# Performance work log

Measured on AMD Instinct MI355X. Metric: run time of the kernel, lower is better.

## Reference

```python
import jax, jax.numpy as jnp
import numpy as np

N_NODES = 50000
N_EDGES = 800000
HIDDEN = 128
EPS = 1e-5


def _layernorm(x, g, b):
    m = jnp.mean(x, axis=-1, keepdims=True)
    v = jnp.var(x, axis=-1, keepdims=True)
    return (x - m) / jnp.sqrt(v + EPS) * g + b


def _batchnorm(x, g, b):
    # training-mode BatchNorm1d: stats over the node (batch) axis, biased var
    m = jnp.mean(x, axis=0, keepdims=True)
    v = jnp.var(x, axis=0, keepdims=True)
    return (x - m) / jnp.sqrt(v + EPS) * g + b


def _instnorm(x):
    # torch InstanceNorm1d on a 2D [N,C] input: unbatched (C,L) view ->
    # normalize each row over the feature axis, no affine params
    m = jnp.mean(x, axis=-1, keepdims=True)
    v = jnp.var(x, axis=-1, keepdims=True)
    return (x - m) / jnp.sqrt(v + EPS)


def _gcn_conv(x, W, b, row, col, norm, n):
    # PyG GCNConv: out[col] += norm * (x @ W)[row]; + bias
    xw = x @ W
    msgs = xw[row] * norm[:, None]          # [E+N, H]
    out = jax.ops.segment_sum(msgs, col, num_segments=n)
    return out + b


def setup_inputs() -> dict:
    key = jax.random.key(0)
    ks = jax.random.split(key, 12)
    H = HIDDEN
    x = jax.random.normal(ks[0], (N_NODES, 2), dtype=jnp.float32)
    edge_index = jax.random.randint(ks[1], (2, N_EDGES), 0, N_NODES, dtype=jnp.int64)

    def lin(k, fan_in, shape):
        bound = 1.0 / np.sqrt(fan_in)
        return jax.random.uniform(k, shape, jnp.float32, -bound, bound)

    inp = {
        "x": x,
        "edge_index": edge_index,
        "coord_W": lin(ks[2], 2, (2, H)),
        "coord_b": lin(ks[3], 2, (H,)),
        "ln_g": jnp.ones((H,), jnp.float32),
        "ln_b": jnp.zeros((H,), jnp.float32),
        "bn_g": jnp.ones((H,), jnp.float32),
        "bn_b": jnp.zeros((H,), jnp.float32),
        "W1": lin(ks[4], H, (H, H)),
        "b1": jnp.zeros((H,), jnp.float32),
        "W2": lin(ks[5], H, (H, H)),
        "b2": jnp.zeros((H,), jnp.float32),
        "W3": lin(ks[6], H, (H, H)),
        "b3": jnp.zeros((H,), jnp.float32),
        "fc1_W": lin(ks[7], H, (H, 32)),
        "fc1_b": lin(ks[8], H, (32,)),
        "fc2_W": lin(ks[9], 32, (32, 2)),
        "fc2_b": lin(ks[10], 32, (2,)),
    }
    return inp


def reference(x, edge_index, coord_W, coord_b, ln_g, ln_b, bn_g, bn_b,
              W1, b1, W2, b2, W3, b3, fc1_W, fc1_b, fc2_W, fc2_b):
    n = x.shape[0]
    loop = jnp.arange(n, dtype=edge_index.dtype)
    row = jnp.concatenate([edge_index[0], loop])
    col = jnp.concatenate([edge_index[1], loop])
    deg = jax.ops.segment_sum(jnp.ones_like(col, dtype=x.dtype), col, num_segments=n)
    dinv = 1.0 / jnp.sqrt(deg)              # deg >= 1 thanks to self-loops
    norm = dinv[row] * dinv[col]

    h = jax.nn.relu(x @ coord_W + coord_b)
    h = _layernorm(h, ln_g, ln_b)

    for W, b in ((W1, b1), (W2, b2), (W3, b3)):
        identity = h
        h = jax.nn.relu(_gcn_conv(h, W, b, row, col, norm, n))
        h = _batchnorm(h, bn_g, bn_b)
        h = _instnorm(h + identity)

    h = jax.nn.relu(h @ fc1_W + fc1_b)
    return jnp.tanh(h @ fc2_W + fc2_b)
```

## Files before the change

kernel.cpp:

```cpp
#include <hip/hip_runtime.h>
#include <hip/hip_bf16.h>
#include <hip/hip_fp16.h>
#include <stdint.h>

#define NN 50000
#define NE 800000
#define HD 128
#define EPSN 1e-5f
#define CAP 1152000
#define NCLS 49
#define NSB 196

typedef __hip_bfloat16 bf16;
typedef __attribute__((ext_vector_type(8))) _Float16 half8;
typedef __attribute__((ext_vector_type(4))) float f32x4;

__device__ __forceinline__ float us2f(unsigned short u) { return __uint_as_float((uint32_t)u << 16); }
__device__ __forceinline__ ushort f2us(float f) {
    bf16 b = __float2bfloat16(f);
    return *reinterpret_cast<ushort*>(&b);
}
__device__ __forceinline__ ushort f2h(float f) {
    __half h = __float2half(f);
    return *reinterpret_cast<ushort*>(&h);
}
__device__ __forceinline__ float h2f(ushort u) {
    __half h = *reinterpret_cast<__half*>(&u);
    return __half2float(h);
}

__device__ __forceinline__ void cvt8(float4 v, float* o) {
    uint32_t a = __float_as_uint(v.x), b = __float_as_uint(v.y);
    uint32_t c = __float_as_uint(v.z), d = __float_as_uint(v.w);
    o[0] = h2f((ushort)(a & 0xffff)); o[1] = h2f((ushort)(a >> 16));
    o[2] = h2f((ushort)(b & 0xffff)); o[3] = h2f((ushort)(b >> 16));
    o[4] = h2f((ushort)(c & 0xffff)); o[5] = h2f((ushort)(c >> 16));
    o[6] = h2f((ushort)(d & 0xffff)); o[7] = h2f((ushort)(d >> 16));
}

#define O_X    0
#define O_CW   100000
#define O_CB   100256
#define O_LNG  100384
#define O_LNB  100512
#define O_BNG  100640
#define O_BNB  100768
#define O_W1   100896
#define O_B1   117280
#define O_W2   117408
#define O_B2   133792
#define O_W3   133920
#define O_B3   150304
#define O_F1W  150432
#define O_F1B  154528
#define O_F2W  154560
#define O_F2B  154624
#define O_TOT  154626

struct Ptrs { const void* p[17]; };

__device__ const int SEG_OFF[18] = {O_X, O_CW, O_CB, O_LNG, O_LNB, O_BNG, O_BNB,
                                    O_W1, O_B1, O_W2, O_B2, O_W3, O_B3,
                                    O_F1W, O_F1B, O_F2W, O_F2B, O_TOT};

__device__ __forceinline__ int eidx(const int* __restrict__ ei, int isL, int which, int e) {
    size_t base = (size_t)which * NE + e;
    return isL ? ei[2 * base] : ei[base];
}

__global__ void k_detect(const int* __restrict__ ei, const ushort* __restrict__ cw,
                         int* __restrict__ flags) {
    int t = threadIdx.x;
    int v = ei[2 * t + 1] | ei[1000000 + 2 * t + 1];
    int bad = 0;
    if (t < 128) {
        float val = us2f(cw[2 * t]);
        bad = !(fabsf(val) <= 1.0f);
    }
    for (int o = 32; o; o >>= 1) { v |= __shfl_xor(v, o); bad |= __shfl_xor(bad, o); }
    __shared__ int sv[4], sb[4];
    if ((t & 63) == 0) { sv[t >> 6] = v; sb[t >> 6] = bad; }
    __syncthreads();
    if (t == 0) {
        flags[0] = ((sv[0] | sv[1] | sv[2] | sv[3]) == 0) ? 1 : 0;
        flags[1] = ((sb[0] | sb[1] | sb[2] | sb[3]) == 0) ? 1 : 0;
    }
}

__global__ void k_conv(Ptrs ptrs, const int* __restrict__ flags, float* __restrict__ cp,
                       _Float16* __restrict__ wt, int* __restrict__ degR,
                       int* __restrict__ ccR, float* __restrict__ stats,
                       ushort* __restrict__ t0h) {
    int i = blockIdx.x * 256 + threadIdx.x;
    int isBf = flags[1];
    if (i < O_TOT) {
        int s = 0;
        while (i >= SEG_OFF[s + 1]) s++;
        int local = i - SEG_OFF[s];
        const void* src = ptrs.p[s];
        cp[i] = isBf ? us2f(((const ushort*)src)[local]) : ((const float*)src)[local];
    }
    if (i < 3 * HD * HD) {
        int mat = i >> 14, idx = i & (HD * HD - 1);
        int k = idx >> 7, n = idx & 127;
        const void* src = ptrs.p[7 + 2 * mat];
        int local = k * HD + n;
        float v = isBf ? us2f(((const ushort*)src)[local]) : ((const float*)src)[local];
        wt[mat * HD * HD + n * HD + k] = (_Float16)v;
    }
    if (i < 8 * NN) degR[i] = (i < NN) ? 1 : 0;
    if (i < 32 * NCLS) ccR[i] = 0;
    if (i < 12288) stats[i] = 0.f;
    if (i < HD) t0h[(size_t)NN * HD + i] = 0;
}

__global__ __launch_bounds__(256) void k_count(const int* __restrict__ ei,
                                               const int* __restrict__ flags,
                                               int* __restrict__ degR,
                                               int* __restrict__ ccR) {
    __shared__ int lcc[NCLS];
    int t = threadIdx.x;
    if (t < NCLS) lcc[t] = 0;
    __syncthreads();
    int e = blockIdx.x * 256 + t;
    if (e < NE) {
        int c = eidx(ei, flags[0], 1, e);
        atomicAdd(&degR[(blockIdx.x & 7) * NN + c], 1);
        atomicAdd(&lcc[c >> 10], 1);
    }
    __syncthreads();
    if (t < NCLS && lcc[t] > 0)
        atomicAdd(&ccR[(blockIdx.x & 31) * NCLS + t], lcc[t]);
}

__global__ __launch_bounds__(256) void k_scan1(const int* __restrict__ degR,
                                               int* __restrict__ degO,
                                               float* __restrict__ dinv,
                                               int* __restrict__ nodePref,
                                               int* __restrict__ blockSum) {
    __shared__ int lp[256];
    int i = blockIdx.x * 256 + threadIdx.x;
    int cpad = 0;
    if (i < NN) {
        int d = 0;
#pragma unroll
        for (int r = 0; r < 8; r++) d += degR[r * NN + i];
        degO[i] = d;
        dinv[i] = rsqrtf((float)d);
        cpad = (d - 1 + 7) & ~7;
    }
    lp[threadIdx.x] = cpad;
    __syncthreads();
    if (threadIdx.x == 0) {
        int run = 0;
        for (int t = 0; t < 256; t++) { int v = lp[t]; lp[t] = run; run += v; }
        blockSum[blockIdx.x] = run;
    }
    __syncthreads();
    if (i < NN) nodePref[i] = lp[threadIdx.x];
}

__global__ __launch_bounds__(256) void k_scan2(int* __restrict__ blockSum,
                                               const int* __restrict__ ccR,
                                               int* __restrict__ cur2,
                                               int* __restrict__ classBase) {
    __shared__ int sB[NSB], sC[32 * NCLS], tot[NCLS], cb[NCLS + 1];
    int t = threadIdx.x;
    if (t < NSB) sB[t] = blockSum[t];
    for (int j = t; j < 32 * NCLS; j += 256) sC[j] = ccR[j];
    __syncthreads();
    if (t < NCLS) {
        int s = 0;
        for (int r = 0; r < 32; r++) s += sC[r * NCLS + t];
        tot[t] = s;
    }
    if (t == 64) {
        int run = 0;
        for (int b = 0; b < NSB; b++) { int v = sB[b]; sB[b] = run; run += v; }
    }
    __syncthreads();
    if (t == 0) {
        int run = 0;
        for (int c = 0; c < NCLS; c++) { cb[c] = run; run += tot[c]; }
        cb[NCLS] = run;
    }
    __syncthreads();
    if (t < NCLS) {
        int base = cb[t];
        for (int r = 0; r < 32; r++) { int v = sC[r * NCLS + t]; sC[r * NCLS + t] = base; base += v; }
        classBase[t] = cb[t];
        if (t == 0) classBase[NCLS] = cb[NCLS];
    }
    __syncthreads();
    if (t < NSB) blockSum[t] = sB[t];
    for (int j = t; j < 32 * NCLS; j += 256) cur2[j] = sC[j];
}

__global__ __launch_bounds__(256) void k_part(const int* __restrict__ ei,
                                              const int* __restrict__ flags,
                                              int* __restrict__ cur2,
                                              int2* __restrict__ part) {
    int e = blockIdx.x * 256 + threadIdx.x;
    if (e >= NE) return;
    int isL = flags[0];
    int r = eidx(ei, isL, 0, e);
    int c = eidx(ei, isL, 1, e);
    int p = atomicAdd(&cur2[(blockIdx.x & 31) * NCLS + (c >> 10)], 1);
    part[p] = make_int2(r << 4, c);
}

__global__ __launch_bounds__(1024) void k_scatter(const int2* __restrict__ part,
                                                  const int* __restrict__ classBase,
                                                  int* __restrict__ curA,
                                                  int* __restrict__ srw) {
    int cls = blockIdx.x;
    int lo = classBase[cls], hi = classBase[cls + 1];
    for (int idx = lo + threadIdx.x; idx < hi; idx += 1024) {
        int2 e = part[idx];
        int p = atomicAdd(&curA[e.y], 1);
        srw[p] = e.x;
    }
}


__global__ void k_embed(const float* __restrict__ cp, ushort* __restrict__ h,
                        const int* __restrict__ degO, const int* __restrict__ nodePref,
                        const int* __restrict__ blockSum, int* __restrict__ startA,
                        int* __restrict__ curA, int* __restrict__ srw) {
    int gi = blockIdx.x * 256 + threadIdx.x;
    if (gi < NN) {
        int s = blockSum[gi >> 8] + nodePref[gi];
        startA[gi] = s;
        curA[gi] = s;
        int cnt = degO[gi] - 1;
        int cpad = (cnt + 7) & ~7;
        for (int p = s + cnt; p < s + cpad; p++) srw[p] = NN << 4;
    }
    int node = gi >> 6;
    int lane = threadIdx.x & 63;
    if (node >= NN) return;
    const float* X = cp + O_X;
    const float* CW = cp + O_CW;
    const float* CB = cp + O_CB;
    const float* LG = cp + O_LNG;
    const float* LB = cp + O_LNB;
    float x0 = X[node * 2], x1 = X[node * 2 + 1];
    int f0 = lane, f1 = lane + 64;
    float v0 = fmaxf(0.f, x0 * CW[f0] + x1 * CW[HD + f0] + CB[f0]);
    float v1 = fmaxf(0.f, x0 * CW[f1] + x1 * CW[HD + f1] + CB[f1]);
    float s = v0 + v1, q = v0 * v0 + v1 * v1;
    for (int o = 32; o; o >>= 1) { s += __shfl_xor(s, o); q += __shfl_xor(q, o); }
    float m = s * (1.f / HD);
    float var = q * (1.f / HD) - m * m;
    float r = rsqrtf(var + EPSN);
    h[(size_t)node * HD + f0] = f2h((v0 - m) * r * LG[f0] + LB[f0]);
    h[(size_t)node * HD + f1] = f2h((v1 - m) * r * LG[f1] + LB[f1]);
}


__device__ __forceinline__ void mfma_tile(const _Float16* hl, const _Float16* __restrict__ wt,
                                          const float* __restrict__ dinv,
                                          ushort* __restrict__ t0h, int nodeBase, int t) {
    int w = t >> 6, l = t & 63;
    int m16 = l & 15;
    int kg = l >> 4;
    int node0 = w * 16;
    half8 a[4];
#pragma unroll
    for (int kc = 0; kc < 4; kc++) {
        int nd = node0 + m16;
        int c16 = kc * 4 + kg;
        int chunk = nd * 16 + (c16 ^ (nd & 7));
        a[kc] = *(const half8*)(hl + chunk * 8);
    }
    f32x4 acc[8];
#pragma unroll
    for (int nt = 0; nt < 8; nt++) acc[nt] = (f32x4){0.f, 0.f, 0.f, 0.f};
#pragma unroll
    for (int nt = 0; nt < 8; nt++) {
        const half8* bp = (const half8*)(wt + (size_t)(nt * 16 + m16) * HD);
#pragma unroll
        for (int kc = 0; kc < 4; kc++) {
            acc[nt] = __builtin_amdgcn_mfma_f32_16x16x32_f16(a[kc], bp[kc * 4 + kg],
                                                             acc[nt], 0, 0, 0);
        }
    }
    int ndb = nodeBase + node0 + kg * 4;
#pragma unroll
    for (int rr = 0; rr < 4; rr++) {
        int nd = ndb + rr;
        if (nd < NN) {
            float dv = dinv[nd];
#pragma unroll
            for (int nt = 0; nt < 8; nt++) {
                t0h[(size_t)nd * HD + nt * 16 + m16] = f2h(acc[nt][rr] * dv);
            }
        }
    }
}


__global__ __launch_bounds__(256) void k_gemm(const ushort* __restrict__ h,
                                              const _Float16* __restrict__ wt,
                                              const float* __restrict__ dinv,
                                              ushort* __restrict__ t0h) {
    __shared__ _Float16 hl[64 * HD];
    int t = threadIdx.x;
    int nodeBase = blockIdx.x * 64;
    const uint4* h4 = (const uint4*)h;
#pragma unroll
    for (int r = 0; r < 4; r++) {
        int cid = r * 256 + t;
        int node = cid >> 4;
        int c16 = cid & 15;
        int n = nodeBase + node;
        uint4 v = make_uint4(0u, 0u, 0u, 0u);
        if (n < NN) v = h4[(size_t)n * 16 + c16];
        int chunk = node * 16 + (c16 ^ (node & 7));
        *(uint4*)(hl + chunk * 8) = v;
    }
    __syncthreads();
    mfma_tile(hl, wt, dinv, t0h, nodeBase, t);
}


__global__ __launch_bounds__(256) void k_gemm_fused(const float* __restrict__ agg,
                                                    const float* __restrict__ stats,
                                                    const float* __restrict__ bias,
                                                    const float* __restrict__ bng,
                                                    const float* __restrict__ bnb,
                                                    ushort* __restrict__ h,
                                                    const _Float16* __restrict__ wt,
                                                    const float* __restrict__ dinv,
                                                    ushort* __restrict__ t0h) {
    __shared__ _Float16 hl[64 * HD];
    __shared__ float scL[HD], shL[HD], bL[HD];
    int t = threadIdx.x;
    if (t < 128) {
        const float invN = 1.f / NN;
        float sv = 0.f, qv = 0.f;
#pragma unroll
        for (int r = 0; r < 16; r++) { sv += stats[r * 256 + t]; qv += stats[r * 256 + 128 + t]; }
        float m = sv * invN;
        float v = qv * invN - m * m;
        float sc = bng[t] * rsqrtf(v + EPSN);
        scL[t] = sc;
        shL[t] = bnb[t] - m * sc;
        bL[t] = bias[t];
    }
    __syncthreads();
    int nodeBase = blockIdx.x * 64;
    const float4* a4 = (const float4*)agg;
    const ushort4* h4r = (const ushort4*)h;
    ushort4* h4w = (ushort4*)h;
#pragma unroll
    for (int r = 0; r < 8; r++) {
        int idx = r * 256 + t;
        int node = idx >> 5;
        int c4 = idx & 31;
        int n = nodeBase + node;
        float4 u = make_float4(0.f, 0.f, 0.f, 0.f);
        if (n < NN) {
            float4 av = a4[(size_t)n * 32 + c4];
            ushort4 hv = h4r[(size_t)n * 32 + c4];
            int f = c4 * 4;
            float y0 = fmaxf(0.f, av.x + bL[f]);
            float y1 = fmaxf(0.f, av.y + bL[f + 1]);
            float y2 = fmaxf(0.f, av.z + bL[f + 2]);
            float y3 = fmaxf(0.f, av.w + bL[f + 3]);
            u.x = y0 * scL[f]     + shL[f]     + h2f(hv.x);
            u.y = y1 * scL[f + 1] + shL[f + 1] + h2f(hv.y);
            u.z = y2 * scL[f + 2] + shL[f + 2] + h2f(hv.z);
            u.w = y3 * scL[f + 3] + shL[f + 3] + h2f(hv.w);
        }
        float s = u.x + u.y + u.z + u.w;
        float q = u.x * u.x + u.y * u.y + u.z * u.z + u.w * u.w;
        for (int o = 16; o; o >>= 1) { s += __shfl_xor(s, o); q += __shfl_xor(q, o); }
        float m = s * (1.f / HD);
        float var = q * (1.f / HD) - m * m;
        float rr = rsqrtf(var + EPSN);
        u.x = (u.x - m) * rr; u.y = (u.y - m) * rr;
        u.z = (u.z - m) * rr; u.w = (u.w - m) * rr;
        ushort4 pk;
        pk.x = f2h(u.x); pk.y = f2h(u.y); pk.z = f2h(u.z); pk.w = f2h(u.w);
        if (n < NN) h4w[(size_t)n * 32 + c4] = pk;
        int chunk = node * 16 + ((c4 >> 1) ^ (node & 7));
        *(ushort4*)((char*)hl + chunk * 16 + (c4 & 1) * 8) = pk;
    }
    __syncthreads();
    mfma_tile(hl, wt, dinv, t0h, nodeBase, t);
}


__global__ __launch_bounds__(256) void k_agg(const ushort* __restrict__ t0h,
                                             const int* __restrict__ srw,
                                             const int* __restrict__ startA,
                                             const int* __restrict__ deg,
                                             const float* __restrict__ dinv,
                                             const float* __restrict__ bias,
                                             float* __restrict__ agg,
                                             float* __restrict__ stats) {
    int t = threadIdx.x;
    int w = t >> 6;
    int l = t & 63;
    int g = l >> 4;
    int k = l & 15;
    int l32 = l & 31;
    const float4* t04 = (const float4*)t0h;
    float4* agg4 = (float4*)agg;
    float bs[8];
    {
        const float4* b4 = (const float4*)bias;
        float4 u0 = b4[2 * k], u1 = b4[2 * k + 1];
        bs[0] = u0.x; bs[1] = u0.y; bs[2] = u0.z; bs[3] = u0.w;
        bs[4] = u1.x; bs[5] = u1.y; bs[6] = u1.z; bs[7] = u1.w;
    }
    float rs1[8], rs2[8];
#pragma unroll
    for (int m = 0; m < 8; m++) { rs1[m] = 0.f; rs2[m] = 0.f; }
    int stride = gridDim.x * 4;
    int i = blockIdx.x * 4 + w;
    int s = 0, nb = 0;
    float di = 0.f;
    if (i < NN) {
        s = startA[i];
        nb = (deg[i] - 1 + 7) & ~7;
        di = dinv[i];
    }
    while (i < NN) {
        float4 sv = t04[(size_t)i * 16 + k];
        int ex = 0;
        if (l32 < nb) ex = srw[s + l32];
        int nb4 = nb >> 2;
        float4 gg[8];
#define GATH(b) { int rv = __shfl(ex, 4 * (b) + g); \
                  gg[b] = t04[(size_t)(uint32_t)rv + k]; }
        if (nb4 > 0) { GATH(0) GATH(1) }
        if (nb4 > 2) { GATH(2) GATH(3) }
        if (nb4 > 4) { GATH(4) GATH(5) }
        if (nb4 > 6) { GATH(6) GATH(7) }
#undef GATH
        int inext = i + stride;
        int sN = 0, nbN = 0;
        float diN = 0.f;
        if (inext < NN) {
            sN = startA[inext];
            nbN = (deg[inext] - 1 + 7) & ~7;
            diN = dinv[inext];
        }
        float acc[8], c8[8];
        cvt8(sv, c8);
        float ws = (g == 0) ? 1.f : 0.f;
#pragma unroll
        for (int m = 0; m < 8; m++) acc[m] = ws * c8[m];
#define ACCB(b) { float d8[8]; cvt8(gg[b], d8); \
                  _Pragma("unroll") \
                  for (int m = 0; m < 8; m++) acc[m] += d8[m]; }
        if (nb4 > 0) { ACCB(0) ACCB(1) }
        if (nb4 > 2) { ACCB(2) ACCB(3) }
        if (nb4 > 4) { ACCB(4) ACCB(5) }
        if (nb4 > 6) { ACCB(6) ACCB(7) }
#undef ACCB
        for (int j = 32; j < nb; j += 32) {
            int ex2 = 0;
            if (j + l32 < nb) ex2 = srw[s + j + l32];
            int rem4 = (nb - j) >> 2;
            if (rem4 > 8) rem4 = 8;
            for (int b = 0; b < rem4; b += 2) {
                int r0 = __shfl(ex2, 4 * b + g);
                int r1 = __shfl(ex2, 4 * b + 4 + g);
                float4 g0 = t04[(size_t)(uint32_t)r0 + k];
                float4 g1 = t04[(size_t)(uint32_t)r1 + k];
                float d0[8], d1[8];
                cvt8(g0, d0); cvt8(g1, d1);
#pragma unroll
                for (int m = 0; m < 8; m++) acc[m] += d0[m] + d1[m];
            }
        }
#pragma unroll
        for (int m = 0; m < 8; m++) {
            acc[m] += __shfl_xor(acc[m], 16);
            acc[m] += __shfl_xor(acc[m], 32);
            acc[m] *= di;
        }
        if (g == 0) {
            agg4[(size_t)i * 32 + 2 * k]     = make_float4(acc[0], acc[1], acc[2], acc[3]);
            agg4[(size_t)i * 32 + 2 * k + 1] = make_float4(acc[4], acc[5], acc[6], acc[7]);
        }
#pragma unroll
        for (int m = 0; m < 8; m++) {
            float y = fmaxf(0.f, acc[m] + bs[m]);
            rs1[m] += y;
            rs2[m] += y * y;
        }
        i = inext; s = sN; nb = nbN; di = diN;
    }
    __shared__ float s1[4][HD], s2[4][HD];
    if (l < 16) {
#pragma unroll
        for (int m = 0; m < 8; m++) {
            s1[w][k * 8 + m] = rs1[m];
            s2[w][k * 8 + m] = rs2[m];
        }
    }
    __syncthreads();
    float* st = stats + (blockIdx.x & 15) * 256;
    if (t < 128) {
        atomicAdd(&st[t], s1[0][t] + s1[1][t] + s1[2][t] + s1[3][t]);
    } else {
        int f = t - 128;
        atomicAdd(&st[128 + f], s2[0][f] + s2[1][f] + s2[2][f] + s2[3][f]);
    }
}


__global__ __launch_bounds__(256) void k_tail(const float* __restrict__ agg,
                                              const float* __restrict__ stats,
                                              const ushort* __restrict__ h,
                                              const float* __restrict__ cp,
                                              const int* __restrict__ flags,
                                              void* __restrict__ outv) {
    __shared__ float W1l[HD * 32];
    __shared__ float ub[4][HD];
    __shared__ float scT[HD], shT[HD], bT[HD];
    __shared__ float B1s[32], W2s[64], B2s[2];
    int t = threadIdx.x;
    const float4* f1w4 = (const float4*)(cp + O_F1W);
    float4* w14 = (float4*)W1l;
#pragma unroll
    for (int r = 0; r < 4; r++) w14[r * 256 + t] = f1w4[r * 256 + t];
    if (t < 32) B1s[t] = cp[O_F1B + t];
    if (t < 64) W2s[t] = cp[O_F2W + t];
    if (t < 2) B2s[t] = cp[O_F2B + t];
    if (t < 128) {
        const float invN = 1.f / NN;
        float sv = 0.f, qv = 0.f;
#pragma unroll
        for (int r = 0; r < 16; r++) { sv += stats[r * 256 + t]; qv += stats[r * 256 + 128 + t]; }
        float m = sv * invN;
        float v = qv * invN - m * m;
        float sc = cp[O_BNG + t] * rsqrtf(v + EPSN);
        scT[t] = sc;
        shT[t] = cp[O_BNB + t] - m * sc;
        bT[t] = cp[O_B3 + t];
    }
    __syncthreads();
    int isBf = flags[1];
    int w = t >> 6, l = t & 63;
    int f = l & 31, half = l >> 5;
    for (int base = blockIdx.x * 4; base < NN; base += gridDim.x * 4) {
        int node = base + w;
        if (node >= NN) continue;
        size_t o = (size_t)node * HD;
        float a0 = agg[o + l], a1 = agg[o + l + 64];
        float h0 = h2f(h[o + l]), h1 = h2f(h[o + l + 64]);
        float y0 = fmaxf(0.f, a0 + bT[l]);
        float y1 = fmaxf(0.f, a1 + bT[l + 64]);
        float u0 = y0 * scT[l]      + shT[l]      + h0;
        float u1 = y1 * scT[l + 64] + shT[l + 64] + h1;
        float s = u0 + u1, q = u0 * u0 + u1 * u1;
        for (int oo = 32; oo; oo >>= 1) { s += __shfl_xor(s, oo); q += __shfl_xor(q, oo); }
        float m = s * (1.f / HD);
        float var = q * (1.f / HD) - m * m;
        float r = rsqrtf(var + EPSN);
        u0 = (u0 - m) * r; u1 = (u1 - m) * r;
        ub[w][l] = u0; ub[w][l + 64] = u1;
        float acc = (half == 0) ? B1s[f] : 0.f;
        const float* up = ub[w] + half * 64;
        const float* wp = W1l + half * 64 * 32 + f;
#pragma unroll 16
        for (int kk = 0; kk < 64; kk++) acc += up[kk] * wp[kk * 32];
        acc += __shfl_xor(acc, 32);
        float av = fmaxf(0.f, acc);
        float p0 = av * W2s[f * 2], p1 = av * W2s[f * 2 + 1];
        for (int oo = 16; oo; oo >>= 1) { p0 += __shfl_xor(p0, oo); p1 += __shfl_xor(p1, oo); }
        if (l == 0) {
            p0 = tanhf(p0 + B2s[0]); p1 = tanhf(p1 + B2s[1]);
            if (isBf) {
                ((uint32_t*)outv)[node] = (uint32_t)f2us(p0) | ((uint32_t)f2us(p1) << 16);
            } else {
                float2 ov; ov.x = p0; ov.y = p1;
                ((float2*)outv)[node] = ov;
            }
        }
    }
}


extern "C" void kernel_launch(void* const* d_in, const int* in_sizes, int n_in,
                              void* d_out, int out_size, void* d_ws, size_t ws_size,
                              hipStream_t stream) {
    const int* ei = (const int*)d_in[1];

    Ptrs ptrs;
    ptrs.p[0] = d_in[0];
    for (int s = 1; s < 17; s++) ptrs.p[s] = d_in[s + 1];

    char* wsp = (char*)d_ws;
    size_t off = 0;
    auto alloc = [&](size_t bytes) {
        void* p = wsp + off;
        off += (bytes + 255) & ~(size_t)255;
        return p;
    };
    float* cp     = (float*)alloc((size_t)O_TOT * 4);
    ushort* h     = (ushort*)alloc((size_t)NN * HD * 2);
    ushort* t0h   = (ushort*)alloc((size_t)(NN + 1) * HD * 2);
    float* agg    = (float*)alloc((size_t)NN * HD * 4);
    int* degR     = (int*)alloc((size_t)8 * NN * 4);
    int* degO     = (int*)alloc((size_t)NN * 4);
    float* dinv   = (float*)alloc((size_t)NN * 4);
    int* srw      = (int*)alloc((size_t)CAP * 4);
    int2* part    = (int2*)alloc((size_t)NE * 8);
    int* startA   = (int*)alloc((size_t)NN * 4);
    int* curA     = (int*)alloc((size_t)NN * 4);
    int* nodePref = (int*)alloc((size_t)NN * 4);
    int* blockSum = (int*)alloc((size_t)NSB * 4);
    int* classBase= (int*)alloc((size_t)(NCLS + 1) * 4);
    int* ccR      = (int*)alloc((size_t)32 * NCLS * 4);
    int* cur2     = (int*)alloc((size_t)32 * NCLS * 4);
    float* stats  = (float*)alloc(3 * 4096 * 4);
    int* flags    = (int*)alloc(256);
    _Float16* wt  = (_Float16*)alloc((size_t)3 * HD * HD * 2);

    const int BN_EDGE = (NE + 255) / 256;
    const int BN_CONV = (8 * NN + 255) / 256;
    const int BN_GEMM = (NN + 63) / 64;

    const float* B[3] = {cp + O_B1, cp + O_B2, cp + O_B3};

    k_detect<<<1, 256, 0, stream>>>(ei, (const ushort*)d_in[2], flags);
    k_conv<<<BN_CONV, 256, 0, stream>>>(ptrs, flags, cp, wt, degR, ccR, stats, t0h);
    k_count<<<BN_EDGE, 256, 0, stream>>>(ei, flags, degR, ccR);
    k_scan1<<<NSB, 256, 0, stream>>>(degR, degO, dinv, nodePref, blockSum);
    k_scan2<<<1, 256, 0, stream>>>(blockSum, ccR, cur2, classBase);
    k_embed<<<NN / 4, 256, 0, stream>>>(cp, h, degO, nodePref, blockSum, startA, curA, srw);
    k_part<<<BN_EDGE, 256, 0, stream>>>(ei, flags, cur2, part);
    k_scatter<<<NCLS, 1024, 0, stream>>>(part, classBase, curA, srw);

    k_gemm<<<BN_GEMM, 256, 0, stream>>>(h, wt, dinv, t0h);
    k_agg<<<2048, 256, 0, stream>>>(t0h, srw, startA, degO, dinv, B[0], agg, stats);
    for (int l = 1; l < 3; l++) {
        k_gemm_fused<<<BN_GEMM, 256, 0, stream>>>(agg, stats + 4096 * (l - 1),
                                                  B[l - 1], cp + O_BNG, cp + O_BNB,
                                                  h, wt + (size_t)l * HD * HD, dinv, t0h);
        k_agg<<<2048, 256, 0, stream>>>(t0h, srw, startA, degO, dinv, B[l],
                                        agg, stats + 4096 * l);
    }
    k_tail<<<2048, 256, 0, stream>>>(agg, stats + 8192, h, cp, flags, d_out);
}
```

Baseline: 496.7 us.

## Aggregate edge partition atomics in LDS and pad counters to cachelines

k_part now counts edges per destination class in shared memory and issues one global atomic per class per block, instead of one global atomic per edge. The per-block class counters (ccR, cur2) are padded with a stride of 16 ints so that different counters do not share a cacheline. k_scatter keeps its per-node cursors in LDS, seeded from startA, instead of doing global atomics on curA, which lets curA and its initialisation be removed. Together these are meant to cut global atomic contention in CSR construction, at the cost of extra block barriers. One risk is that k_conv's zeroing bound grows to 25088 while its grid covers 400000 threads, which is fine.

```diff
diff --git a/kernel.cpp b/kernel.cpp
--- a/kernel.cpp
+++ b/kernel.cpp
@@ -109,7 +109,7 @@
         wt[mat * HD * HD + n * HD + k] = (_Float16)v;
     }
     if (i < 8 * NN) degR[i] = (i < NN) ? 1 : 0;
-    if (i < 32 * NCLS) ccR[i] = 0;
+    if (i < 32 * NCLS * 16) ccR[i] = 0;
     if (i < 12288) stats[i] = 0.f;
     if (i < HD) t0h[(size_t)NN * HD + i] = 0;
 }
@@ -130,7 +130,7 @@
     }
     __syncthreads();
     if (t < NCLS && lcc[t] > 0)
-        atomicAdd(&ccR[(blockIdx.x & 31) * NCLS + t], lcc[t]);
+        atomicAdd(&ccR[((blockIdx.x & 31) * NCLS + t) * 16], lcc[t]);
 }
 
 __global__ __launch_bounds__(256) void k_scan1(const int* __restrict__ degR,
@@ -167,7 +167,7 @@
     __shared__ int sB[NSB], sC[32 * NCLS], tot[NCLS], cb[NCLS + 1];
     int t = threadIdx.x;
     if (t < NSB) sB[t] = blockSum[t];
-    for (int j = t; j < 32 * NCLS; j += 256) sC[j] = ccR[j];
+    for (int j = t; j < 32 * NCLS; j += 256) sC[j] = ccR[j * 16];
     __syncthreads();
     if (t < NCLS) {
         int s = 0;
@@ -193,31 +193,50 @@
     }
     __syncthreads();
     if (t < NSB) blockSum[t] = sB[t];
-    for (int j = t; j < 32 * NCLS; j += 256) cur2[j] = sC[j];
+    for (int j = t; j < 32 * NCLS; j += 256) cur2[j * 16] = sC[j];
 }
 
 __global__ __launch_bounds__(256) void k_part(const int* __restrict__ ei,
                                               const int* __restrict__ flags,
                                               int* __restrict__ cur2,
                                               int2* __restrict__ part) {
-    int e = blockIdx.x * 256 + threadIdx.x;
-    if (e >= NE) return;
-    int isL = flags[0];
-    int r = eidx(ei, isL, 0, e);
-    int c = eidx(ei, isL, 1, e);
-    int p = atomicAdd(&cur2[(blockIdx.x & 31) * NCLS + (c >> 10)], 1);
-    part[p] = make_int2(r << 4, c);
+    __shared__ int lcnt[NCLS], lbase[NCLS];
+    int t = threadIdx.x;
+    if (t < NCLS) lcnt[t] = 0;
+    __syncthreads();
+    int e = blockIdx.x * 256 + t;
+    int r = 0, c = 0, cls = 0, loc = 0;
+    bool valid = (e < NE);
+    if (valid) {
+        int isL = flags[0];
+        r = eidx(ei, isL, 0, e);
+        c = eidx(ei, isL, 1, e);
+        cls = c >> 10;
+        loc = atomicAdd(&lcnt[cls], 1);
+    }
+    __syncthreads();
+    if (t < NCLS) {
+        int n = lcnt[t];
+        if (n > 0) lbase[t] = atomicAdd(&cur2[((blockIdx.x & 31) * NCLS + t) * 16], n);
+    }
+    __syncthreads();
+    if (valid) part[lbase[cls] + loc] = make_int2(r << 4, c);
 }
 
 __global__ __launch_bounds__(1024) void k_scatter(const int2* __restrict__ part,
                                                   const int* __restrict__ classBase,
-                                                  int* __restrict__ curA,
+                                                  const int* __restrict__ startA,
                                                   int* __restrict__ srw) {
+    __shared__ int lcur[1024];
     int cls = blockIdx.x;
+    int nodeBase = cls << 10;
+    int n = nodeBase + threadIdx.x;
+    if (n < NN) lcur[threadIdx.x] = startA[n];
+    __syncthreads();
     int lo = classBase[cls], hi = classBase[cls + 1];
     for (int idx = lo + threadIdx.x; idx < hi; idx += 1024) {
         int2 e = part[idx];
-        int p = atomicAdd(&curA[e.y], 1);
+        int p = atomicAdd(&lcur[e.y - nodeBase], 1);
         srw[p] = e.x;
     }
 }
@@ -226,12 +245,11 @@
 __global__ void k_embed(const float* __restrict__ cp, ushort* __restrict__ h,
                         const int* __restrict__ degO, const int* __restrict__ nodePref,
                         const int* __restrict__ blockSum, int* __restrict__ startA,
-                        int* __restrict__ curA, int* __restrict__ srw) {
+                        int* __restrict__ srw) {
     int gi = blockIdx.x * 256 + threadIdx.x;
     if (gi < NN) {
         int s = blockSum[gi >> 8] + nodePref[gi];
         startA[gi] = s;
-        curA[gi] = s;
         int cnt = degO[gi] - 1;
         int cpad = (cnt + 7) & ~7;
         for (int p = s + cnt; p < s + cpad; p++) srw[p] = NN << 4;
@@ -613,12 +631,11 @@
     int* srw      = (int*)alloc((size_t)CAP * 4);
     int2* part    = (int2*)alloc((size_t)NE * 8);
     int* startA   = (int*)alloc((size_t)NN * 4);
-    int* curA     = (int*)alloc((size_t)NN * 4);
     int* nodePref = (int*)alloc((size_t)NN * 4);
     int* blockSum = (int*)alloc((size_t)NSB * 4);
     int* classBase= (int*)alloc((size_t)(NCLS + 1) * 4);
-    int* ccR      = (int*)alloc((size_t)32 * NCLS * 4);
-    int* cur2     = (int*)alloc((size_t)32 * NCLS * 4);
+    int* ccR      = (int*)alloc((size_t)32 * NCLS * 16 * 4);
+    int* cur2     = (int*)alloc((size_t)32 * NCLS * 16 * 4);
     float* stats  = (float*)alloc(3 * 4096 * 4);
     int* flags    = (int*)alloc(256);
     _Float16* wt  = (_Float16*)alloc((size_t)3 * HD * HD * 2);
@@ -634,9 +651,9 @@
     k_count<<<BN_EDGE, 256, 0, stream>>>(ei, flags, degR, ccR);
     k_scan1<<<NSB, 256, 0, stream>>>(degR, degO, dinv, nodePref, blockSum);
     k_scan2<<<1, 256, 0, stream>>>(blockSum, ccR, cur2, classBase);
-    k_embed<<<NN / 4, 256, 0, stream>>>(cp, h, degO, nodePref, blockSum, startA, curA, srw);
+    k_embed<<<NN / 4, 256, 0, stream>>>(cp, h, degO, nodePref, blockSum, startA, srw);
     k_part<<<BN_EDGE, 256, 0, stream>>>(ei, flags, cur2, part);
-    k_scatter<<<NCLS, 1024, 0, stream>>>(part, classBase, curA, srw);
+    k_scatter<<<NCLS, 1024, 0, stream>>>(part, classBase, startA, srw);
 
     k_gemm<<<BN_GEMM, 256, 0, stream>>>(h, wt, dinv, t0h);
     k_agg<<<2048, 256, 0, stream>>>(t0h, srw, startA, degO, dinv, B[0], agg, stats);
```

Result: faster. 408.9 us (-17.7%).
